# Kernel optimization log

Measured on AMD Instinct MI355X. Metric: run time of the kernel, lower is better.

Reference implementation:

```python
import jax, jax.numpy as jnp
import numpy as np

N_IN, N_OUT = 1024, 4096
D_IN = 1024          # next power of two of N_IN (no padding needed)
STACK = 4            # ceil(N_OUT / D_IN)
BATCH = 8192


def fwht0(x):
    """Unnormalized fast Walsh-Hadamard transform along axis 0 of a (D, C) matrix."""
    D, C = x.shape
    h = 1
    while h < D:
        y = x.reshape(D // (2 * h), 2, h, C)
        a, b = y[:, 0], y[:, 1]
        x = jnp.stack([a + b, a - b], axis=1).reshape(D, C)
        h *= 2
    return x


def sample_block(s1, s2, g_mu, g_rho, eps):
    # W = diag(s1) @ H @ diag(g_tilde) @ H @ diag(s2)
    g_tilde = g_mu + jax.nn.softplus(g_rho) * eps            # (D,)
    Hs2 = fwht0(jnp.diag(s2))                                # H @ diag(s2)
    W = s1[:, None] * fwht0(g_tilde[:, None] * Hs2)          # (D, D)
    return W


def setup_inputs() -> dict:
    key = jax.random.key(0)
    k = jax.random.split(key, 6)
    return {
        "x": jax.random.normal(k[0], (BATCH, N_IN), dtype=jnp.float32),
        "s1": jax.random.normal(k[1], (STACK, D_IN), dtype=jnp.float32),
        "s2": jax.random.normal(k[2], (STACK, D_IN), dtype=jnp.float32),
        "g_mu": jax.random.normal(k[3], (STACK, D_IN), dtype=jnp.float32),
        "g_rho": jax.random.uniform(k[4], (STACK, D_IN), dtype=jnp.float32) - 3.0,
        "eps": jax.random.normal(k[5], (STACK, D_IN), dtype=jnp.float32),
    }


def reference(x, s1, s2, g_mu, g_rho, eps):
    # Sample all stacked square blocks and concatenate rows -> (D_out, D_in)
    Ws = jax.vmap(sample_block)(s1, s2, g_mu, g_rho, eps)    # (stack, D, D)
    W = Ws.reshape(STACK * D_IN, D_IN)                       # (D_out, D_in)
    # Pad input to D_in (no-op here since N_IN == D_IN, kept for fidelity)
    x_padded = jnp.pad(x, ((0, 0), (0, D_IN - N_IN)))
    out = x_padded @ W.T                                     # (B, D_out)
    return out[..., :N_OUT]
```

## Files before the change

### kernel.cpp

```cpp
#include <hip/hip_runtime.h>
#include <math.h>

#define D_IN   1024
#define STACKN 4
#define BATCHN 8192
#define OUTW   (STACKN * D_IN)

typedef int iv2 __attribute__((ext_vector_type(2)));

__device__ __forceinline__ int   f2i(float x){ union{float f;int i;}u; u.f=x; return u.i; }
__device__ __forceinline__ float i2f(int x){ union{float f;int i;}u; u.i=x; return u.f; }

template<int CTRL>
__device__ __forceinline__ float dpp_mov(float v){
    return i2f(__builtin_amdgcn_update_dpp(0, f2i(v), CTRL, 0xF, 0xF, false));
}

__device__ __forceinline__ void fwht1024(float v[16],
                                         float sg1, float sg2,
                                         float sg4, float sg8)
{
    #pragma unroll
    for (int m = 1; m <= 8; m <<= 1) {
        #pragma unroll
        for (int r = 0; r < 16; ++r) {
            if (!(r & m)) {
                float a = v[r], b = v[r ^ m];
                v[r]     = a + b;
                v[r ^ m] = a - b;
            }
        }
    }

    #pragma unroll
    for (int r = 0; r < 16; ++r) {
        float t = dpp_mov<0xB1>(v[r]);
        v[r] = fmaf(v[r], sg1, t);
    }
    #pragma unroll
    for (int r = 0; r < 16; ++r) {
        float t = dpp_mov<0x4E>(v[r]);
        v[r] = fmaf(v[r], sg2, t);
    }
    #pragma unroll
    for (int r = 0; r < 16; ++r) {
        float t = i2f(__builtin_amdgcn_ds_swizzle(f2i(v[r]), 0x101F));
        v[r] = fmaf(v[r], sg4, t);
    }
    #pragma unroll
    for (int r = 0; r < 16; ++r) {
        float t = dpp_mov<0x128>(v[r]);
        v[r] = fmaf(v[r], sg8, t);
    }
    #pragma unroll
    for (int r = 0; r < 16; r += 2) {
        iv2 p = __builtin_amdgcn_permlane16_swap(f2i(v[r]), f2i(v[r+1]), false, false);
        float a = i2f(p[0]), b = i2f(p[1]);
        float s = a + b, d = a - b;
        iv2 q = __builtin_amdgcn_permlane16_swap(f2i(s), f2i(d), false, false);
        v[r]   = i2f(q[0]);
        v[r+1] = i2f(q[1]);
    }
    #pragma unroll
    for (int r = 0; r < 16; r += 2) {
        iv2 p = __builtin_amdgcn_permlane32_swap(f2i(v[r]), f2i(v[r+1]), false, false);
        float a = i2f(p[0]), b = i2f(p[1]);
        float s = a + b, d = a - b;
        iv2 q = __builtin_amdgcn_permlane32_swap(f2i(s), f2i(d), false, false);
        v[r]   = i2f(q[0]);
        v[r+1] = i2f(q[1]);
    }
}

__global__ __launch_bounds__(256) void whvi_prep(
    const float* __restrict__ g_mu, const float* __restrict__ g_rho,
    const float* __restrict__ eps, float* __restrict__ gt)
{
    const int i = blockIdx.x * 256 + threadIdx.x;
    const float r  = g_rho[i];
    const float sp = fmaxf(r, 0.0f) + log1pf(expf(-fabsf(r)));
    gt[i] = fmaf(sp, eps[i], g_mu[i]);
}

template<bool USE_WS>
__global__ __launch_bounds__(256) void whvi_main(
    const float* __restrict__ x,
    const float* __restrict__ s1,
    const float* __restrict__ s2,
    const float* __restrict__ g_mu,
    const float* __restrict__ g_rho,
    const float* __restrict__ eps,
    const float* __restrict__ gt,
    float* __restrict__ out)
{
    const int lane = threadIdx.x & 63;
    const int row  = (blockIdx.x << 2) + (threadIdx.x >> 6);

    const float sg1 = (lane & 1) ? -1.0f : 1.0f;
    const float sg2 = (lane & 2) ? -1.0f : 1.0f;
    const float sg4 = (lane & 4) ? -1.0f : 1.0f;
    const float sg8 = (lane & 8) ? -1.0f : 1.0f;

    const float* __restrict__ xr = x + (size_t)row * D_IN;
    float xv[16];
    #pragma unroll
    for (int k = 0; k < 4; ++k) {
        float4 t = *(const float4*)(xr + (k << 8) + (lane << 2));
        xv[k*4+0] = t.x; xv[k*4+1] = t.y; xv[k*4+2] = t.z; xv[k*4+3] = t.w;
    }

    float* __restrict__ orow = out + (size_t)row * OUTW;

    #pragma unroll
    for (int s = 0; s < STACKN; ++s) {
        const int pb = s * D_IN + (lane << 2);
        float s2v[16], gv[16], s1v[16], v[16];
        #pragma unroll
        for (int k = 0; k < 4; ++k) {
            float4 t2 = *(const float4*)(s2 + pb + (k << 8));
            s2v[k*4+0] = t2.x; s2v[k*4+1] = t2.y; s2v[k*4+2] = t2.z; s2v[k*4+3] = t2.w;
            float4 t1 = *(const float4*)(s1 + pb + (k << 8));
            s1v[k*4+0] = t1.x; s1v[k*4+1] = t1.y; s1v[k*4+2] = t1.z; s1v[k*4+3] = t1.w;
            if (USE_WS) {
                float4 tg = *(const float4*)(gt + pb + (k << 8));
                gv[k*4+0] = tg.x; gv[k*4+1] = tg.y; gv[k*4+2] = tg.z; gv[k*4+3] = tg.w;
            } else {
                #pragma unroll
                for (int c = 0; c < 4; ++c) {
                    const int i = pb + (k << 8) + c;
                    const float rr = g_rho[i];
                    const float sp = fmaxf(rr, 0.0f) + log1pf(expf(-fabsf(rr)));
                    gv[k*4+c] = fmaf(sp, eps[i], g_mu[i]);
                }
            }
        }

        #pragma unroll
        for (int r = 0; r < 16; ++r) v[r] = xv[r] * s2v[r];

        fwht1024(v, sg1, sg2, sg4, sg8);

        #pragma unroll
        for (int r = 0; r < 16; ++r) v[r] *= gv[r];

        fwht1024(v, sg1, sg2, sg4, sg8);

        #pragma unroll
        for (int k = 0; k < 4; ++k) {
            float4 t = make_float4(v[k*4+0] * s1v[k*4+0],
                                   v[k*4+1] * s1v[k*4+1],
                                   v[k*4+2] * s1v[k*4+2],
                                   v[k*4+3] * s1v[k*4+3]);
            *(float4*)(orow + s * D_IN + (k << 8) + (lane << 2)) = t;
        }
    }
}

extern "C" void kernel_launch(void* const* d_in, const int* in_sizes, int n_in,
                              void* d_out, int out_size, void* d_ws, size_t ws_size,
                              hipStream_t stream) {
    const float* x     = (const float*)d_in[0];
    const float* s1    = (const float*)d_in[1];
    const float* s2    = (const float*)d_in[2];
    const float* g_mu  = (const float*)d_in[3];
    const float* g_rho = (const float*)d_in[4];
    const float* eps   = (const float*)d_in[5];
    float* out = (float*)d_out;

    const bool use_ws = ws_size >= (size_t)(STACKN * D_IN * sizeof(float));
    if (use_ws) {
        float* gt = (float*)d_ws;
        whvi_prep<<<STACKN * D_IN / 256, 256, 0, stream>>>(g_mu, g_rho, eps, gt);
        whvi_main<true><<<BATCHN / 4, 256, 0, stream>>>(x, s1, s2, g_mu, g_rho, eps, gt, out);
    } else {
        whvi_main<false><<<BATCHN / 4, 256, 0, stream>>>(x, s1, s2, g_mu, g_rho, eps, nullptr, out);
    }
}
```

Measured before the change: 178.5 us.

## Process two batch rows per wave with interleaved FWHTs and nontemporal stores

Each wavefront now transforms two input rows at once. The two FWHT chains are interleaved to raise instruction-level parallelism, and the loads of s1, s2 and g_tilde are shared across both rows. The lane-bit-4 butterfly uses a ds_swizzle xor-16 with a sign FMA in place of the permlane16_swap pair. Output stores become nontemporal, launch bounds gain a min-blocks hint, and the grid is halved. In exchange, register pressure roughly doubles, which could limit occupancy or cause spills.

```diff
diff --git a/kernel.cpp b/kernel.cpp
--- a/kernel.cpp
+++ b/kernel.cpp
@@ -6,7 +6,8 @@
 #define BATCHN 8192
 #define OUTW   (STACKN * D_IN)
 
-typedef int iv2 __attribute__((ext_vector_type(2)));
+typedef int   iv2 __attribute__((ext_vector_type(2)));
+typedef float fv4 __attribute__((ext_vector_type(4)));
 
 __device__ __forceinline__ int   f2i(float x){ union{float f;int i;}u; u.f=x; return u.i; }
 __device__ __forceinline__ float i2f(int x){ union{float f;int i;}u; u.i=x; return u.f; }
@@ -16,59 +17,67 @@
     return i2f(__builtin_amdgcn_update_dpp(0, f2i(v), CTRL, 0xF, 0xF, false));
 }
 
-__device__ __forceinline__ void fwht1024(float v[16],
-                                         float sg1, float sg2,
-                                         float sg4, float sg8)
+__device__ __forceinline__ void fwht1024x2(float a[16], float b[16],
+                                           float sg1, float sg2, float sg4,
+                                           float sg8, float sg16)
 {
     #pragma unroll
     for (int m = 1; m <= 8; m <<= 1) {
         #pragma unroll
         for (int r = 0; r < 16; ++r) {
             if (!(r & m)) {
-                float a = v[r], b = v[r ^ m];
-                v[r]     = a + b;
-                v[r ^ m] = a - b;
+                float x0 = a[r], x1 = a[r ^ m];
+                a[r] = x0 + x1;  a[r ^ m] = x0 - x1;
+                float y0 = b[r], y1 = b[r ^ m];
+                b[r] = y0 + y1;  b[r ^ m] = y0 - y1;
             }
         }
     }
-
-    #pragma unroll
-    for (int r = 0; r < 16; ++r) {
-        float t = dpp_mov<0xB1>(v[r]);
-        v[r] = fmaf(v[r], sg1, t);
-    }
-    #pragma unroll
-    for (int r = 0; r < 16; ++r) {
-        float t = dpp_mov<0x4E>(v[r]);
-        v[r] = fmaf(v[r], sg2, t);
-    }
-    #pragma unroll
-    for (int r = 0; r < 16; ++r) {
-        float t = i2f(__builtin_amdgcn_ds_swizzle(f2i(v[r]), 0x101F));
-        v[r] = fmaf(v[r], sg4, t);
-    }
-    #pragma unroll
-    for (int r = 0; r < 16; ++r) {
-        float t = dpp_mov<0x128>(v[r]);
-        v[r] = fmaf(v[r], sg8, t);
+    #pragma unroll
+    for (int r = 0; r < 16; ++r) {
+        float ta = dpp_mov<0xB1>(a[r]); a[r] = fmaf(a[r], sg1, ta);
+        float tb = dpp_mov<0xB1>(b[r]); b[r] = fmaf(b[r], sg1, tb);
+    }
+    #pragma unroll
+    for (int r = 0; r < 16; ++r) {
+        float ta = dpp_mov<0x4E>(a[r]); a[r] = fmaf(a[r], sg2, ta);
+        float tb = dpp_mov<0x4E>(b[r]); b[r] = fmaf(b[r], sg2, tb);
+    }
+    #pragma unroll
+    for (int r = 0; r < 16; ++r) {
+        float ta = i2f(__builtin_amdgcn_ds_swizzle(f2i(a[r]), 0x101F));
+        float tb = i2f(__builtin_amdgcn_ds_swizzle(f2i(b[r]), 0x101F));
+        a[r] = fmaf(a[r], sg4, ta);
+        b[r] = fmaf(b[r], sg4, tb);
+    }
+    #pragma unroll
+    for (int r = 0; r < 16; ++r) {
+        float ta = dpp_mov<0x128>(a[r]); a[r] = fmaf(a[r], sg8, ta);
+        float tb = dpp_mov<0x128>(b[r]); b[r] = fmaf(b[r], sg8, tb);
+    }
+    #pragma unroll
+    for (int r = 0; r < 16; ++r) {
+        float ta = i2f(__builtin_amdgcn_ds_swizzle(f2i(a[r]), 0x401F));
+        float tb = i2f(__builtin_amdgcn_ds_swizzle(f2i(b[r]), 0x401F));
+        a[r] = fmaf(a[r], sg16, ta);
+        b[r] = fmaf(b[r], sg16, tb);
     }
     #pragma unroll
     for (int r = 0; r < 16; r += 2) {
-        iv2 p = __builtin_amdgcn_permlane16_swap(f2i(v[r]), f2i(v[r+1]), false, false);
-        float a = i2f(p[0]), b = i2f(p[1]);
-        float s = a + b, d = a - b;
-        iv2 q = __builtin_amdgcn_permlane16_swap(f2i(s), f2i(d), false, false);
-        v[r]   = i2f(q[0]);
-        v[r+1] = i2f(q[1]);
-    }
-    #pragma unroll
-    for (int r = 0; r < 16; r += 2) {
-        iv2 p = __builtin_amdgcn_permlane32_swap(f2i(v[r]), f2i(v[r+1]), false, false);
-        float a = i2f(p[0]), b = i2f(p[1]);
-        float s = a + b, d = a - b;
-        iv2 q = __builtin_amdgcn_permlane32_swap(f2i(s), f2i(d), false, false);
-        v[r]   = i2f(q[0]);
-        v[r+1] = i2f(q[1]);
+        {
+            iv2 p = __builtin_amdgcn_permlane32_swap(f2i(a[r]), f2i(a[r+1]), false, false);
+            float u = i2f(p[0]), w = i2f(p[1]);
+            float sum = u + w, dif = u - w;
+            iv2 q = __builtin_amdgcn_permlane32_swap(f2i(sum), f2i(dif), false, false);
+            a[r] = i2f(q[0]); a[r+1] = i2f(q[1]);
+        }
+        {
+            iv2 p = __builtin_amdgcn_permlane32_swap(f2i(b[r]), f2i(b[r+1]), false, false);
+            float u = i2f(p[0]), w = i2f(p[1]);
+            float sum = u + w, dif = u - w;
+            iv2 q = __builtin_amdgcn_permlane32_swap(f2i(sum), f2i(dif), false, false);
+            b[r] = i2f(q[0]); b[r+1] = i2f(q[1]);
+        }
     }
 }
 
@@ -83,7 +92,7 @@
 }
 
 template<bool USE_WS>
-__global__ __launch_bounds__(256) void whvi_main(
+__global__ __launch_bounds__(256, 4) void whvi_main(
     const float* __restrict__ x,
     const float* __restrict__ s1,
     const float* __restrict__ s2,
@@ -94,35 +103,40 @@
     float* __restrict__ out)
 {
     const int lane = threadIdx.x & 63;
-    const int row  = (blockIdx.x << 2) + (threadIdx.x >> 6);
-
-    const float sg1 = (lane & 1) ? -1.0f : 1.0f;
-    const float sg2 = (lane & 2) ? -1.0f : 1.0f;
-    const float sg4 = (lane & 4) ? -1.0f : 1.0f;
-    const float sg8 = (lane & 8) ? -1.0f : 1.0f;
-
-    const float* __restrict__ xr = x + (size_t)row * D_IN;
-    float xv[16];
+    const int row0 = (((blockIdx.x << 2) + (threadIdx.x >> 6)) << 1);
+
+    const float sg1  = (lane & 1)  ? -1.0f : 1.0f;
+    const float sg2  = (lane & 2)  ? -1.0f : 1.0f;
+    const float sg4  = (lane & 4)  ? -1.0f : 1.0f;
+    const float sg8  = (lane & 8)  ? -1.0f : 1.0f;
+    const float sg16 = (lane & 16) ? -1.0f : 1.0f;
+
+    const float* __restrict__ xr0 = x + (size_t)row0 * D_IN;
+    const float* __restrict__ xr1 = xr0 + D_IN;
+    float xa[16], xb[16];
     #pragma unroll
     for (int k = 0; k < 4; ++k) {
-        float4 t = *(const float4*)(xr + (k << 8) + (lane << 2));
-        xv[k*4+0] = t.x; xv[k*4+1] = t.y; xv[k*4+2] = t.z; xv[k*4+3] = t.w;
-    }
-
-    float* __restrict__ orow = out + (size_t)row * OUTW;
+        fv4 t0 = *(const fv4*)(xr0 + (k << 8) + (lane << 2));
+        xa[k*4+0] = t0.x; xa[k*4+1] = t0.y; xa[k*4+2] = t0.z; xa[k*4+3] = t0.w;
+        fv4 t1 = *(const fv4*)(xr1 + (k << 8) + (lane << 2));
+        xb[k*4+0] = t1.x; xb[k*4+1] = t1.y; xb[k*4+2] = t1.z; xb[k*4+3] = t1.w;
+    }
+
+    float* __restrict__ orow0 = out + (size_t)row0 * OUTW;
+    float* __restrict__ orow1 = orow0 + OUTW;
 
     #pragma unroll
     for (int s = 0; s < STACKN; ++s) {
         const int pb = s * D_IN + (lane << 2);
-        float s2v[16], gv[16], s1v[16], v[16];
+        float s2v[16], gv[16], s1v[16];
         #pragma unroll
         for (int k = 0; k < 4; ++k) {
-            float4 t2 = *(const float4*)(s2 + pb + (k << 8));
+            fv4 t2 = *(const fv4*)(s2 + pb + (k << 8));
             s2v[k*4+0] = t2.x; s2v[k*4+1] = t2.y; s2v[k*4+2] = t2.z; s2v[k*4+3] = t2.w;
-            float4 t1 = *(const float4*)(s1 + pb + (k << 8));
+            fv4 t1 = *(const fv4*)(s1 + pb + (k << 8));
             s1v[k*4+0] = t1.x; s1v[k*4+1] = t1.y; s1v[k*4+2] = t1.z; s1v[k*4+3] = t1.w;
             if (USE_WS) {
-                float4 tg = *(const float4*)(gt + pb + (k << 8));
+                fv4 tg = *(const fv4*)(gt + pb + (k << 8));
                 gv[k*4+0] = tg.x; gv[k*4+1] = tg.y; gv[k*4+2] = tg.z; gv[k*4+3] = tg.w;
             } else {
                 #pragma unroll
@@ -135,23 +149,31 @@
             }
         }
 
-        #pragma unroll
-        for (int r = 0; r < 16; ++r) v[r] = xv[r] * s2v[r];
-
-        fwht1024(v, sg1, sg2, sg4, sg8);
-
-        #pragma unroll
-        for (int r = 0; r < 16; ++r) v[r] *= gv[r];
-
-        fwht1024(v, sg1, sg2, sg4, sg8);
+        float va[16], vb[16];
+        #pragma unroll
+        for (int r = 0; r < 16; ++r) { va[r] = xa[r] * s2v[r]; vb[r] = xb[r] * s2v[r]; }
+
+        fwht1024x2(va, vb, sg1, sg2, sg4, sg8, sg16);
+
+        #pragma unroll
+        for (int r = 0; r < 16; ++r) { va[r] *= gv[r]; vb[r] *= gv[r]; }
+
+        fwht1024x2(va, vb, sg1, sg2, sg4, sg8, sg16);
 
         #pragma unroll
         for (int k = 0; k < 4; ++k) {
-            float4 t = make_float4(v[k*4+0] * s1v[k*4+0],
-                                   v[k*4+1] * s1v[k*4+1],
-                                   v[k*4+2] * s1v[k*4+2],
-                                   v[k*4+3] * s1v[k*4+3]);
-            *(float4*)(orow + s * D_IN + (k << 8) + (lane << 2)) = t;
+            fv4 ta;
+            ta.x = va[k*4+0] * s1v[k*4+0];
+            ta.y = va[k*4+1] * s1v[k*4+1];
+            ta.z = va[k*4+2] * s1v[k*4+2];
+            ta.w = va[k*4+3] * s1v[k*4+3];
+            __builtin_nontemporal_store(ta, (fv4*)(orow0 + s * D_IN + (k << 8) + (lane << 2)));
+            fv4 tb;
+            tb.x = vb[k*4+0] * s1v[k*4+0];
+            tb.y = vb[k*4+1] * s1v[k*4+1];
+            tb.z = vb[k*4+2] * s1v[k*4+2];
+            tb.w = vb[k*4+3] * s1v[k*4+3];
+            __builtin_nontemporal_store(tb, (fv4*)(orow1 + s * D_IN + (k << 8) + (lane << 2)));
         }
     }
 }
@@ -171,8 +193,8 @@
     if (use_ws) {
         float* gt = (float*)d_ws;
         whvi_prep<<<STACKN * D_IN / 256, 256, 0, stream>>>(g_mu, g_rho, eps, gt);
-        whvi_main<true><<<BATCHN / 4, 256, 0, stream>>>(x, s1, s2, g_mu, g_rho, eps, gt, out);
+        whvi_main<true><<<BATCHN / 8, 256, 0, stream>>>(x, s1, s2, g_mu, g_rho, eps, gt, out);
     } else {
-        whvi_main<false><<<BATCHN / 4, 256, 0, stream>>>(x, s1, s2, g_mu, g_rho, eps, nullptr, out);
-    }
-}
+        whvi_main<false><<<BATCHN / 8, 256, 0, stream>>>(x, s1, s2, g_mu, g_rho, eps, nullptr, out);
+    }
+}
```

Result: slower. 188.4 us (+5.5%).

## Split work by stack across grid and process multiple rows per wave with prefetch

Applied to the files above, without the earlier changes.

Each wave now handles one stack block for four consecutive batch rows instead of all four stacks for one row, with the stack index on grid y. Per-stack parameters (s1, s2, g_tilde) are loaded once per wave and reused across rows, and the next x row is prefetched into registers while the current row is transformed. The cost is that each x row is read by four different blocks, relying on cache, and register pressure rises from the double-buffered row.

```diff
diff --git a/kernel.cpp b/kernel.cpp
--- a/kernel.cpp
+++ b/kernel.cpp
@@ -5,8 +5,10 @@
 #define STACKN 4
 #define BATCHN 8192
 #define OUTW   (STACKN * D_IN)
-
-typedef int iv2 __attribute__((ext_vector_type(2)));
+#define ROWS_PER_WAVE 4
+
+typedef int   iv2 __attribute__((ext_vector_type(2)));
+typedef float fv4 __attribute__((ext_vector_type(4)));
 
 __device__ __forceinline__ int   f2i(float x){ union{float f;int i;}u; u.f=x; return u.i; }
 __device__ __forceinline__ float i2f(int x){ union{float f;int i;}u; u.i=x; return u.f; }
@@ -31,7 +33,6 @@
             }
         }
     }
-
     #pragma unroll
     for (int r = 0; r < 16; ++r) {
         float t = dpp_mov<0xB1>(v[r]);
@@ -93,50 +94,65 @@
     const float* __restrict__ gt,
     float* __restrict__ out)
 {
-    const int lane = threadIdx.x & 63;
-    const int row  = (blockIdx.x << 2) + (threadIdx.x >> 6);
+    const int lane  = threadIdx.x & 63;
+    const int stack = blockIdx.y;
+    const int wave  = blockIdx.x * 4 + (threadIdx.x >> 6);
+    const int row0  = wave * ROWS_PER_WAVE;
 
     const float sg1 = (lane & 1) ? -1.0f : 1.0f;
     const float sg2 = (lane & 2) ? -1.0f : 1.0f;
     const float sg4 = (lane & 4) ? -1.0f : 1.0f;
     const float sg8 = (lane & 8) ? -1.0f : 1.0f;
 
-    const float* __restrict__ xr = x + (size_t)row * D_IN;
-    float xv[16];
+    const int pb = stack * D_IN + (lane << 2);
+    float s2v[16], gv[16], s1v[16];
     #pragma unroll
     for (int k = 0; k < 4; ++k) {
-        float4 t = *(const float4*)(xr + (k << 8) + (lane << 2));
-        xv[k*4+0] = t.x; xv[k*4+1] = t.y; xv[k*4+2] = t.z; xv[k*4+3] = t.w;
-    }
-
-    float* __restrict__ orow = out + (size_t)row * OUTW;
-
-    #pragma unroll
-    for (int s = 0; s < STACKN; ++s) {
-        const int pb = s * D_IN + (lane << 2);
-        float s2v[16], gv[16], s1v[16], v[16];
+        fv4 t2 = *(const fv4*)(s2 + pb + (k << 8));
+        s2v[k*4+0] = t2.x; s2v[k*4+1] = t2.y; s2v[k*4+2] = t2.z; s2v[k*4+3] = t2.w;
+        fv4 t1 = *(const fv4*)(s1 + pb + (k << 8));
+        s1v[k*4+0] = t1.x; s1v[k*4+1] = t1.y; s1v[k*4+2] = t1.z; s1v[k*4+3] = t1.w;
+        if (USE_WS) {
+            fv4 tg = *(const fv4*)(gt + pb + (k << 8));
+            gv[k*4+0] = tg.x; gv[k*4+1] = tg.y; gv[k*4+2] = tg.z; gv[k*4+3] = tg.w;
+        } else {
+            #pragma unroll
+            for (int c = 0; c < 4; ++c) {
+                const int i = pb + (k << 8) + c;
+                const float rr = g_rho[i];
+                const float sp = fmaxf(rr, 0.0f) + log1pf(expf(-fabsf(rr)));
+                gv[k*4+c] = fmaf(sp, eps[i], g_mu[i]);
+            }
+        }
+    }
+
+    float cur[16];
+    {
+        const float* __restrict__ xr = x + (size_t)row0 * D_IN;
         #pragma unroll
         for (int k = 0; k < 4; ++k) {
-            float4 t2 = *(const float4*)(s2 + pb + (k << 8));
-            s2v[k*4+0] = t2.x; s2v[k*4+1] = t2.y; s2v[k*4+2] = t2.z; s2v[k*4+3] = t2.w;
-            float4 t1 = *(const float4*)(s1 + pb + (k << 8));
-            s1v[k*4+0] = t1.x; s1v[k*4+1] = t1.y; s1v[k*4+2] = t1.z; s1v[k*4+3] = t1.w;
-            if (USE_WS) {
-                float4 tg = *(const float4*)(gt + pb + (k << 8));
-                gv[k*4+0] = tg.x; gv[k*4+1] = tg.y; gv[k*4+2] = tg.z; gv[k*4+3] = tg.w;
-            } else {
-                #pragma unroll
-                for (int c = 0; c < 4; ++c) {
-                    const int i = pb + (k << 8) + c;
-                    const float rr = g_rho[i];
-                    const float sp = fmaxf(rr, 0.0f) + log1pf(expf(-fabsf(rr)));
-                    gv[k*4+c] = fmaf(sp, eps[i], g_mu[i]);
-                }
+            fv4 t = *(const fv4*)(xr + (k << 8) + (lane << 2));
+            cur[k*4+0] = t.x; cur[k*4+1] = t.y; cur[k*4+2] = t.z; cur[k*4+3] = t.w;
+        }
+    }
+
+    #pragma unroll
+    for (int i = 0; i < ROWS_PER_WAVE; ++i) {
+        const int row = row0 + i;
+
+        float nxt[16];
+        if (i < ROWS_PER_WAVE - 1) {
+            const float* __restrict__ xr = x + (size_t)(row + 1) * D_IN;
+            #pragma unroll
+            for (int k = 0; k < 4; ++k) {
+                fv4 t = *(const fv4*)(xr + (k << 8) + (lane << 2));
+                nxt[k*4+0] = t.x; nxt[k*4+1] = t.y; nxt[k*4+2] = t.z; nxt[k*4+3] = t.w;
             }
         }
 
-        #pragma unroll
-        for (int r = 0; r < 16; ++r) v[r] = xv[r] * s2v[r];
+        float v[16];
+        #pragma unroll
+        for (int r = 0; r < 16; ++r) v[r] = cur[r] * s2v[r];
 
         fwht1024(v, sg1, sg2, sg4, sg8);
 
@@ -145,13 +161,20 @@
 
         fwht1024(v, sg1, sg2, sg4, sg8);
 
+        float* __restrict__ orow = out + (size_t)row * OUTW + stack * D_IN;
         #pragma unroll
         for (int k = 0; k < 4; ++k) {
-            float4 t = make_float4(v[k*4+0] * s1v[k*4+0],
-                                   v[k*4+1] * s1v[k*4+1],
-                                   v[k*4+2] * s1v[k*4+2],
-                                   v[k*4+3] * s1v[k*4+3]);
-            *(float4*)(orow + s * D_IN + (k << 8) + (lane << 2)) = t;
+            fv4 t;
+            t.x = v[k*4+0] * s1v[k*4+0];
+            t.y = v[k*4+1] * s1v[k*4+1];
+            t.z = v[k*4+2] * s1v[k*4+2];
+            t.w = v[k*4+3] * s1v[k*4+3];
+            *(fv4*)(orow + (k << 8) + (lane << 2)) = t;
+        }
+
+        if (i < ROWS_PER_WAVE - 1) {
+            #pragma unroll
+            for (int r = 0; r < 16; ++r) cur[r] = nxt[r];
         }
     }
 }
@@ -167,12 +190,14 @@
     const float* eps   = (const float*)d_in[5];
     float* out = (float*)d_out;
 
+    dim3 grid(BATCHN / ROWS_PER_WAVE / 4, STACKN);
+
     const bool use_ws = ws_size >= (size_t)(STACKN * D_IN * sizeof(float));
     if (use_ws) {
         float* gt = (float*)d_ws;
         whvi_prep<<<STACKN * D_IN / 256, 256, 0, stream>>>(g_mu, g_rho, eps, gt);
-        whvi_main<true><<<BATCHN / 4, 256, 0, stream>>>(x, s1, s2, g_mu, g_rho, eps, gt, out);
+        whvi_main<true><<<grid, 256, 0, stream>>>(x, s1, s2, g_mu, g_rho, eps, gt, out);
     } else {
-        whvi_main<false><<<BATCHN / 4, 256, 0, stream>>>(x, s1, s2, g_mu, g_rho, eps, nullptr, out);
-    }
-}
+        whvi_main<false><<<grid, 256, 0, stream>>>(x, s1, s2, g_mu, g_rho, eps, nullptr, out);
+    }
+}
```

Result: slower. 184.2 us (+3.2%).
